# Kernel tuning notes

Measured on AMD Instinct MI355X. Metric: run time of the kernel, lower is better.

Reference implementation:

```python
import jax, jax.numpy as jnp
import numpy as np

SLOPE = 0.2  # LeakyReLU negative slope
EPS = 1e-8


def setup_inputs() -> dict:
    key = jax.random.key(0)
    ks = jax.random.split(key, 10)
    B, LL, D, H = 16, 257, 64, 128
    in_dim = D + 1  # lags=1 -> lags*D + 1
    sc = 0.1
    return {
        "x": jax.random.normal(ks[0], (B, LL, D), dtype=jnp.float32),
        "W1": jax.random.normal(ks[1], (D, H, in_dim), dtype=jnp.float32) * sc,
        "b1": jax.random.normal(ks[2], (D, H), dtype=jnp.float32) * sc,
        "W2": jax.random.normal(ks[3], (D, H, H), dtype=jnp.float32) * sc,
        "b2": jax.random.normal(ks[4], (D, H), dtype=jnp.float32) * sc,
        "W3": jax.random.normal(ks[5], (D, H, H), dtype=jnp.float32) * sc,
        "b3": jax.random.normal(ks[6], (D, H), dtype=jnp.float32) * sc,
        "W4": jax.random.normal(ks[7], (D, 1, H), dtype=jnp.float32) * sc,
        "b4": jax.random.normal(ks[8], (D, 1), dtype=jnp.float32) * sc,
        "lags": 1,
    }


def _forward(x, W1, b1, W2, b2, W3, b3, W4, b4, lags):
    B, LL, D = x.shape
    length = LL - lags
    # sliding windows of size lags+1 along time: [B, length, lags+1, D]
    windows = jnp.stack([x[:, i:i + length] for i in range(lags + 1)], axis=2)
    N = B * length
    x_lags = windows[:, :, :-1].reshape(N, lags * D)  # [N, lags*D]
    x_t = windows[:, :, -1].reshape(N, D)             # [N, D]

    def per_latent(w1, bb1, w2, bb2, w3, bb3, w4, bb4, xti):
        inp = jnp.concatenate([x_lags, xti[:, None]], axis=-1)  # [N, lags*D+1]
        p1 = inp @ w1.T + bb1
        s1 = jnp.where(p1 > 0, 1.0, SLOPE)
        a1 = p1 * s1
        p2 = a1 @ w2.T + bb2
        s2 = jnp.where(p2 > 0, 1.0, SLOPE)
        a2 = p2 * s2
        p3 = a2 @ w3.T + bb3
        s3 = jnp.where(p3 > 0, 1.0, SLOPE)
        a3 = p3 * s3
        out = a3 @ w4.T + bb4  # [N, 1]
        # analytic d out / d x_{t,i} (Jacobian diagonal): chain through LeakyReLU slopes
        d = s1 * w1[:, -1]      # [N, H]
        d = s2 * (d @ w2.T)     # [N, H]
        d = s3 * (d @ w3.T)     # [N, H]
        deriv = d @ w4[0]       # [N]
        return out[:, 0], deriv

    res, deriv = jax.vmap(per_latent, in_axes=(0, 0, 0, 0, 0, 0, 0, 0, 1))(
        W1, b1, W2, b2, W3, b3, W4, b4, x_t)  # res, deriv: [D, N]
    residuals = res.T.reshape(B, length, D)
    log_abs_det = jnp.log(jnp.abs(deriv) + EPS).sum(axis=0).reshape(B, length)
    return residuals, log_abs_det


def reference(x, W1, b1, W2, b2, W3, b3, W4, b4, lags):
    return _forward(x, W1, b1, W2, b2, W3, b3, W4, b4, lags)
```

## Files before the change

kernel.cpp:

```cpp
#include <hip/hip_runtime.h>
#include <hip/hip_bf16.h>
#include <math.h>

typedef _Float16 f16;
typedef _Float16 f16x8 __attribute__((ext_vector_type(8)));
typedef _Float16 f16x4 __attribute__((ext_vector_type(4)));
typedef float f32x4 __attribute__((ext_vector_type(4)));

#define MFMA(a, b, c) __builtin_amdgcn_mfma_f32_16x16x32_f16((a), (b), (c), 0, 0, 0)

constexpr int Dd = 64;
constexpr int Hh = 128;
constexpr int Nn = 4096;
constexpr int NT = 32;
constexpr float SLP = 0.2f;
constexpr float INV2K = 1.0f / 2048.0f;

constexpr int PD = 81920;
constexpr size_t W1L_OFF = (size_t)Dd * PD * 2;
constexpr size_t WS_NEEDED = W1L_OFF + (size_t)Dd * Hh * 4;

__device__ __forceinline__ int swz(int r, int c) {
  return (r << 7) + ((((c >> 3) ^ (r & 15)) << 3) | (c & 7));
}
__device__ __forceinline__ int swzK64(int r, int c) {
  return (r << 6) + (((((c >> 3) ^ r) & 7) << 3) | (c & 7));
}
__device__ __forceinline__ int swzF(int n, int h) {
  return (n << 7) + ((((h >> 2) ^ n) & 31) << 2) + (h & 3);
}

struct HL { f16 h, l; };
__device__ __forceinline__ HL split(float v) {
  HL r;
  r.h = (f16)v;
  r.l = (f16)((v - (float)r.h) * 2048.0f);
  return r;
}

__device__ __forceinline__ void cp_lds_async512(const void* g, void* l, int nbytes, int tid) {
  const int lane = tid & 63, wv = tid >> 6;
  for (int base = wv * 1024; base < nbytes; base += 8192) {
    __builtin_amdgcn_global_load_lds(
        (const __attribute__((address_space(1))) void*)((const char*)g + base + lane * 16),
        (__attribute__((address_space(3))) void*)((char*)l + base), 16, 0, 0);
  }
}

__global__ __launch_bounds__(256)
void prep_kernel(const float* __restrict__ W1, const float* __restrict__ W2,
                 const float* __restrict__ W3, f16* __restrict__ wsf,
                 float* __restrict__ w1lg, float* __restrict__ out_log) {
  const int gid = blockIdx.x * 256 + threadIdx.x;
  if (gid < Dd * Hh) w1lg[gid] = W1[(gid >> 7) * 8320 + (gid & 127) * 65 + 64];
  if (gid < Nn) out_log[gid] = 0.f;

  const int d = gid / 10240;
  const int r = gid - d * 10240;
  f16* outd = wsf + (size_t)d * PD;
  float vv[8];
  f16* dst;
  int plane;
  if (r < 2048) {
    int rem = r & 1023;
    int hf = r >> 10;
    plane = rem >> 9;
    int j = rem & 511;
    int row = j >> 3, sc = j & 7;
    int h = hf * 64 + row;
    int k0 = (sc ^ (row & 7)) << 3;
    const float* src = W1 + d * 8320 + h * 65 + k0;
#pragma unroll
    for (int e = 0; e < 8; e++) vv[e] = src[e];
    dst = outd + r * 8;
  } else {
    int r2 = r - 2048;
    int wsec = r2 >> 11;
    int rr = r2 & 2047;
    plane = rr >> 10;
    int j = rr & 1023;
    int row = j >> 4, sc = j & 15;
    int k0 = (sc ^ (row & 15)) << 3;
    const float* base = (wsec < 2 ? W2 : W3) + d * 16384 + (wsec & 1) * 8192;
    const float* src = base + row * 128 + k0;
    float4 v0 = *(const float4*)src, v1 = *(const float4*)(src + 4);
    vv[0] = v0.x; vv[1] = v0.y; vv[2] = v0.z; vv[3] = v0.w;
    vv[4] = v1.x; vv[5] = v1.y; vv[6] = v1.z; vv[7] = v1.w;
    dst = outd + 16384 + (wsec >> 1) * 32768 + (wsec & 1) * 16384 + rr * 8;
  }
  if (plane) {
#pragma unroll
    for (int e = 0; e < 8; e++) {
      f16 hi = (f16)vv[e];
      vv[e] = (vv[e] - (float)hi) * 2048.0f;
    }
  }
  f16x8 o;
#pragma unroll
  for (int e = 0; e < 8; e++) o[e] = (f16)vv[e];
  *(f16x8*)dst = o;
}

__device__ __forceinline__ void mid_phase(const f16* wb,
                                          const f16x8* axh, const f16x8* axl,
                                          const f16x8* ayh, const f16x8* ayl,
                                          int hr, int quad,
                                          f32x4& aP, f32x4& aS, f32x4& dP, f32x4& dS) {
#pragma unroll
  for (int kc = 0; kc < 4; kc++) {
    int ko = kc * 32 + quad * 8;
    f16x8 wh = *(const f16x8*)&wb[swz(hr, ko)];
    f16x8 wl = *(const f16x8*)&wb[8192 + swz(hr, ko)];
    aP = MFMA(wh, axh[kc], aP);
    aS = MFMA(wl, axh[kc], aS);
    aS = MFMA(wh, axl[kc], aS);
    dP = MFMA(wh, ayh[kc], dP);
    dS = MFMA(wl, ayh[kc], dS);
    dS = MFMA(wh, ayl[kc], dS);
  }
}

__global__ __launch_bounds__(512, 4)
void np_prior_fast(const float* __restrict__ x, const f16* __restrict__ wsw,
                   const float* __restrict__ w1lg,
                   const float* __restrict__ b1, const float* __restrict__ b2,
                   const float* __restrict__ b3, const float* __restrict__ W4,
                   const float* __restrict__ b4,
                   float* __restrict__ out_res, float* __restrict__ out_log) {
  __shared__ float4 smem[4096];
  f16* AH = (f16*)smem;
  f16* AL = AH + NT * 128;
  f16* DH = AL + NT * 128;
  f16* DL = DH + NT * 128;
  f16* Wreg = (f16*)((char*)smem + 32768);
  float* A3F = (float*)smem;
  float* D3F = (float*)((char*)smem + 16384);

  const int tid = threadIdx.x, d = blockIdx.y, n0 = blockIdx.x * NT;
  const int lane = tid & 63, wv = tid >> 6, l15 = lane & 15, quad = lane >> 4;
  const int nt = wv & 1, wq = wv >> 1;
  const int ra = nt * 16 + l15;
  const int hr = wq * 16 + l15;

  const f16* wd = wsw + (size_t)d * PD;
  const float* w1l = w1lg + d * Hh;
  const float* b1d = b1 + d * Hh;
  const f32x4 zero = {0.f, 0.f, 0.f, 0.f};

  cp_lds_async512(wd, Wreg, 32768, tid);
  {
    int n = tid >> 4, k4 = (tid & 15) << 2;
    int ng = n0 + n, bb = ng >> 8, tt = ng & 255;
    float4 v = *(const float4*)&x[(bb * 257 + tt) * 64 + k4];
    HL a = split(v.x), b = split(v.y), c = split(v.z), e = split(v.w);
    int o = swz(n, k4);
    *(f16x4*)&AH[o] = f16x4{a.h, b.h, c.h, e.h};
    *(f16x4*)&AL[o] = f16x4{a.l, b.l, c.l, e.l};
  }
  float xtv;
  {
    int ng = n0 + ra, bb = ng >> 8, tt = ng & 255;
    xtv = x[(bb * 257 + tt + 1) * 64 + d];
  }
  __syncthreads();

  f32x4 l1P[2], l1S[2];
  {
    f16x8 l1xh[2], l1xl[2];
#pragma unroll
    for (int kc = 0; kc < 2; kc++) {
      int ko = kc * 32 + quad * 8;
      l1xh[kc] = *(const f16x8*)&AH[swz(ra, ko)];
      l1xl[kc] = *(const f16x8*)&AL[swz(ra, ko)];
    }
#pragma unroll
    for (int hf = 0; hf < 2; hf++) {
      const f16* wb = Wreg + hf * 8192;
      l1P[hf] = zero; l1S[hf] = zero;
#pragma unroll
      for (int kc = 0; kc < 2; kc++) {
        int ko = kc * 32 + quad * 8;
        f16x8 wh = *(const f16x8*)&wb[swzK64(hr, ko)];
        f16x8 wl = *(const f16x8*)&wb[4096 + swzK64(hr, ko)];
        l1P[hf] = MFMA(wh, l1xh[kc], l1P[hf]);
        l1S[hf] = MFMA(wl, l1xh[kc], l1S[hf]);
        l1S[hf] = MFMA(wh, l1xl[kc], l1S[hf]);
      }
    }
  }
  __syncthreads();
  cp_lds_async512(wd + 16384, Wreg, 32768, tid);

#pragma unroll
  for (int hf = 0; hf < 2; hf++) {
    int hb = hf * 64 + wq * 16 + quad * 4;
    float4 wv4 = *(const float4*)&w1l[hb];
    float4 bv4 = *(const float4*)&b1d[hb];
    f16x4 ah, al, dh, dl;
#pragma unroll
    for (int j = 0; j < 4; j++) {
      float w1j = (&wv4.x)[j];
      float p = l1P[hf][j] + l1S[hf][j] * INV2K + xtv * w1j + (&bv4.x)[j];
      float s = p > 0.f ? 1.f : SLP;
      HL av = split(p * s), dv = split(s * w1j);
      ah[j] = av.h; al[j] = av.l; dh[j] = dv.h; dl[j] = dv.l;
    }
    int o = swz(ra, hb);
    *(f16x4*)&AH[o] = ah; *(f16x4*)&AL[o] = al;
    *(f16x4*)&DH[o] = dh; *(f16x4*)&DL[o] = dl;
  }
  __syncthreads();

  f32x4 aP[2], aS[2], dP[2], dS[2];
  {
    f16x8 axh[4], axl[4], ayh[4], ayl[4];
#pragma unroll
    for (int kc = 0; kc < 4; kc++) {
      int ko = kc * 32 + quad * 8;
      axh[kc] = *(const f16x8*)&AH[swz(ra, ko)];
      axl[kc] = *(const f16x8*)&AL[swz(ra, ko)];
      ayh[kc] = *(const f16x8*)&DH[swz(ra, ko)];
      ayl[kc] = *(const f16x8*)&DL[swz(ra, ko)];
    }
#pragma unroll
    for (int hf = 0; hf < 2; hf++) {
      if (hf == 1) {
        __syncthreads();
        cp_lds_async512(wd + 32768, Wreg, 32768, tid);
        __syncthreads();
      }
      aP[hf] = zero; aS[hf] = zero; dP[hf] = zero; dS[hf] = zero;
      mid_phase(Wreg, axh, axl, ayh, ayl, hr, quad,
                aP[hf], aS[hf], dP[hf], dS[hf]);
    }
  }
  __syncthreads();
  cp_lds_async512(wd + 49152, Wreg, 32768, tid);

  {
    const float* b2d = b2 + d * Hh;
#pragma unroll
    for (int hf = 0; hf < 2; hf++) {
      int hb = hf * 64 + wq * 16 + quad * 4;
      float4 bv4 = *(const float4*)&b2d[hb];
      f16x4 ah, al, dh, dl;
#pragma unroll
      for (int j = 0; j < 4; j++) {
        float p = aP[hf][j] + aS[hf][j] * INV2K + (&bv4.x)[j];
        float s = p > 0.f ? 1.f : SLP;
        float dd = s * (dP[hf][j] + dS[hf][j] * INV2K);
        HL av = split(p * s), dv = split(dd);
        ah[j] = av.h; al[j] = av.l; dh[j] = dv.h; dl[j] = dv.l;
      }
      int o = swz(ra, hb);
      *(f16x4*)&AH[o] = ah; *(f16x4*)&AL[o] = al;
      *(f16x4*)&DH[o] = dh; *(f16x4*)&DL[o] = dl;
    }
  }
  __syncthreads();

  {
    f16x8 axh[4], axl[4], ayh[4], ayl[4];
#pragma unroll
    for (int kc = 0; kc < 4; kc++) {
      int ko = kc * 32 + quad * 8;
      axh[kc] = *(const f16x8*)&AH[swz(ra, ko)];
      axl[kc] = *(const f16x8*)&AL[swz(ra, ko)];
      ayh[kc] = *(const f16x8*)&DH[swz(ra, ko)];
      ayl[kc] = *(const f16x8*)&DL[swz(ra, ko)];
    }
#pragma unroll
    for (int hf = 0; hf < 2; hf++) {
      if (hf == 1) {
        __syncthreads();
        cp_lds_async512(wd + 65536, Wreg, 32768, tid);
        __syncthreads();
      }
      aP[hf] = zero; aS[hf] = zero; dP[hf] = zero; dS[hf] = zero;
      mid_phase(Wreg, axh, axl, ayh, ayl, hr, quad,
                aP[hf], aS[hf], dP[hf], dS[hf]);
    }
  }
  __syncthreads();

  {
    const float* b3d = b3 + d * Hh;
#pragma unroll
    for (int hf = 0; hf < 2; hf++) {
      int hb = hf * 64 + wq * 16 + quad * 4;
      float4 bv4 = *(const float4*)&b3d[hb];
      float4 pa, pd;
#pragma unroll
      for (int j = 0; j < 4; j++) {
        float p = aP[hf][j] + aS[hf][j] * INV2K + (&bv4.x)[j];
        float s = p > 0.f ? 1.f : SLP;
        (&pa.x)[j] = p * s;
        (&pd.x)[j] = s * (dP[hf][j] + dS[hf][j] * INV2K);
      }
      *(float4*)&A3F[swzF(ra, hb)] = pa;
      *(float4*)&D3F[swzF(ra, hb)] = pd;
    }
  }
  __syncthreads();

  {
    int n = tid >> 4, g16 = tid & 15;
    const float* w4d = W4 + d * Hh;
    int c = g16 * 8;
    float4 va0 = *(const float4*)&A3F[swzF(n, c)];
    float4 va1 = *(const float4*)&A3F[swzF(n, c + 4)];
    float4 vd0 = *(const float4*)&D3F[swzF(n, c)];
    float4 vd1 = *(const float4*)&D3F[swzF(n, c + 4)];
    float4 w0 = *(const float4*)&w4d[c];
    float4 w1 = *(const float4*)&w4d[c + 4];
    float sr = va0.x * w0.x + va0.y * w0.y + va0.z * w0.z + va0.w * w0.w +
               va1.x * w1.x + va1.y * w1.y + va1.z * w1.z + va1.w * w1.w;
    float sd = vd0.x * w0.x + vd0.y * w0.y + vd0.z * w0.z + vd0.w * w0.w +
               vd1.x * w1.x + vd1.y * w1.y + vd1.z * w1.z + vd1.w * w1.w;
    sr += __shfl_xor(sr, 1); sr += __shfl_xor(sr, 2);
    sr += __shfl_xor(sr, 4); sr += __shfl_xor(sr, 8);
    sd += __shfl_xor(sd, 1); sd += __shfl_xor(sd, 2);
    sd += __shfl_xor(sd, 4); sd += __shfl_xor(sd, 8);
    if (g16 == 0) {
      int ng = n0 + n;
      out_res[ng * 64 + d] = sr + b4[d];
      atomicAdd(&out_log[ng], logf(fabsf(sd) + 1e-8f));
    }
  }
}

__device__ __forceinline__ void stage_wf(f16* WH, f16* WL,
                                         const float* __restrict__ g, int tid) {
  for (int i = tid; i < 2048; i += 256) {
    int h = i >> 5, k4 = (i & 31) << 2;
    float4 v = ((const float4*)g)[i];
    HL a = split(v.x), b = split(v.y), c = split(v.z), e = split(v.w);
    int o = swz(h, k4);
    *(f16x4*)&WH[o] = f16x4{a.h, b.h, c.h, e.h};
    *(f16x4*)&WL[o] = f16x4{a.l, b.l, c.l, e.l};
  }
}

__device__ __forceinline__ void mid_mfma_half(
    const f16* AH, const f16* AL, const f16* DH, const f16* DL,
    const f16* WH, const f16* WL, int nt, int wq, int l15, int quad,
    f32x4* aP, f32x4* aS, f32x4* dP, f32x4* dS) {
#pragma unroll
  for (int kc = 0; kc < 4; kc++) {
    int ko = kc * 32 + quad * 8;
    int ra = nt * 16 + l15;
    f16x8 xh = *(const f16x8*)&AH[swz(ra, ko)];
    f16x8 xl = *(const f16x8*)&AL[swz(ra, ko)];
    f16x8 yh = *(const f16x8*)&DH[swz(ra, ko)];
    f16x8 yl = *(const f16x8*)&DL[swz(ra, ko)];
#pragma unroll
    for (int c2 = 0; c2 < 2; c2++) {
      int hr = (2 * wq + c2) * 16 + l15;
      f16x8 wh = *(const f16x8*)&WH[swz(hr, ko)];
      f16x8 wl = *(const f16x8*)&WL[swz(hr, ko)];
      aP[c2] = MFMA(wh, xh, aP[c2]);
      aS[c2] = MFMA(wl, xh, aS[c2]);
      aS[c2] = MFMA(wh, xl, aS[c2]);
      dP[c2] = MFMA(wh, yh, dP[c2]);
      dS[c2] = MFMA(wl, yh, dS[c2]);
      dS[c2] = MFMA(wh, yl, dS[c2]);
    }
  }
}

__global__ __launch_bounds__(256, 2)
void np_prior_fb(const float* __restrict__ x,
                 const float* __restrict__ W1, const float* __restrict__ b1,
                 const float* __restrict__ W2, const float* __restrict__ b2,
                 const float* __restrict__ W3, const float* __restrict__ b3,
                 const float* __restrict__ W4, const float* __restrict__ b4,
                 float* __restrict__ out_res, float* __restrict__ out_log) {
  __shared__ float4 smem[4096];
  f16* AH = (f16*)smem;
  f16* AL = AH + NT * 128;
  f16* DH = AL + NT * 128;
  f16* DL = DH + NT * 128;
  f16* WHp = (f16*)((char*)smem + 32768);
  f16* WLp = WHp + 64 * 128;
  float* A3F = (float*)smem;
  float* D3F = (float*)((char*)smem + 16384);

  const int tid = threadIdx.x, d = blockIdx.y, n0 = blockIdx.x * NT;
  const int lane = tid & 63, wv = tid >> 6, l15 = lane & 15, quad = lane >> 4;
  const int nt = wv & 1, wq = wv >> 1;

  const float* W1d = W1 + d * Hh * 65;
  const float* b1d = b1 + d * Hh;
  const f32x4 zero = {0.f, 0.f, 0.f, 0.f};

  for (int i = tid; i < NT * 16; i += 256) {
    int n = i >> 4, k4 = (i & 15) << 2;
    int ng = n0 + n, bb = ng >> 8, tt = ng & 255;
    float4 v = *(const float4*)&x[(bb * 257 + tt) * 64 + k4];
    HL a = split(v.x), b = split(v.y), c = split(v.z), e = split(v.w);
    int o = swz(n, k4);
    *(f16x4*)&AH[o] = f16x4{a.h, b.h, c.h, e.h};
    *(f16x4*)&AL[o] = f16x4{a.l, b.l, c.l, e.l};
  }
  float xtv;
  {
    int ng = n0 + nt * 16 + l15, bb = ng >> 8, tt = ng & 255;
    xtv = x[(bb * 257 + tt + 1) * 64 + d];
  }
  for (int i = tid; i < 64 * 64; i += 256) {
    int h = i >> 6, k = i & 63;
    HL s = split(W1d[h * 65 + k]);
    int o = swz(h, k);
    WHp[o] = s.h; WLp[o] = s.l;
  }
  __syncthreads();

  f32x4 l1P[2][2], l1S[2][2];
  for (int hf = 0; hf < 2; hf++) {
    if (hf == 1) {
      __syncthreads();
      for (int i = tid; i < 64 * 64; i += 256) {
        int h = i >> 6, k = i & 63;
        HL s = split(W1d[(64 + h) * 65 + k]);
        int o = swz(h, k);
        WHp[o] = s.h; WLp[o] = s.l;
      }
      __syncthreads();
    }
    l1P[hf][0] = zero; l1P[hf][1] = zero;
    l1S[hf][0] = zero; l1S[hf][1] = zero;
#pragma unroll
    for (int kc = 0; kc < 2; kc++) {
      int ko = kc * 32 + quad * 8;
      f16x8 xh = *(const f16x8*)&AH[swz(nt * 16 + l15, ko)];
      f16x8 xl = *(const f16x8*)&AL[swz(nt * 16 + l15, ko)];
#pragma unroll
      for (int c2 = 0; c2 < 2; c2++) {
        int hr = (2 * wq + c2) * 16 + l15;
        f16x8 wh = *(const f16x8*)&WHp[swz(hr, ko)];
        f16x8 wl = *(const f16x8*)&WLp[swz(hr, ko)];
        l1P[hf][c2] = MFMA(wh, xh, l1P[hf][c2]);
        l1S[hf][c2] = MFMA(wl, xh, l1S[hf][c2]);
        l1S[hf][c2] = MFMA(wh, xl, l1S[hf][c2]);
      }
    }
  }
  __syncthreads();

  {
    int n = nt * 16 + l15;
#pragma unroll
    for (int hf = 0; hf < 2; hf++)
#pragma unroll
      for (int c2 = 0; c2 < 2; c2++) {
        int hb = hf * 64 + (2 * wq + c2) * 16 + quad * 4;
        f16x4 ah, al, dh, dl;
#pragma unroll
        for (int j = 0; j < 4; j++) {
          int h = hb + j;
          float w1j = W1d[h * 65 + 64];
          float p = l1P[hf][c2][j] + l1S[hf][c2][j] * INV2K + xtv * w1j + b1d[h];
          float s = p > 0.f ? 1.f : SLP;
          HL av = split(p * s), dv = split(s * w1j);
          ah[j] = av.h; al[j] = av.l; dh[j] = dv.h; dl[j] = dv.l;
        }
        int o = swz(n, hb);
        *(f16x4*)&AH[o] = ah; *(f16x4*)&AL[o] = al;
        *(f16x4*)&DH[o] = dh; *(f16x4*)&DL[o] = dl;
      }
  }
  stage_wf(WHp, WLp, W2 + d * Hh * Hh, tid);
  __syncthreads();

  f32x4 aP[2][2], aS[2][2], dP[2][2], dS[2][2];
  for (int hf = 0; hf < 2; hf++) {
    if (hf == 1) {
      __syncthreads();
      stage_wf(WHp, WLp, W2 + d * Hh * Hh + 64 * 128, tid);
      __syncthreads();
    }
    aP[hf][0] = zero; aP[hf][1] = zero; aS[hf][0] = zero; aS[hf][1] = zero;
    dP[hf][0] = zero; dP[hf][1] = zero; dS[hf][0] = zero; dS[hf][1] = zero;
    mid_mfma_half(AH, AL, DH, DL, WHp, WLp, nt, wq, l15, quad,
                  aP[hf], aS[hf], dP[hf], dS[hf]);
  }
  __syncthreads();

  {
    const float* b2d = b2 + d * Hh;
    int n = nt * 16 + l15;
#pragma unroll
    for (int hf = 0; hf < 2; hf++)
#pragma unroll
      for (int c2 = 0; c2 < 2; c2++) {
        int hb = hf * 64 + (2 * wq + c2) * 16 + quad * 4;
        f16x4 ah, al, dh, dl;
#pragma unroll
        for (int j = 0; j < 4; j++) {
          int h = hb + j;
          float p = aP[hf][c2][j] + aS[hf][c2][j] * INV2K + b2d[h];
          float s = p > 0.f ? 1.f : SLP;
          float dd = s * (dP[hf][c2][j] + dS[hf][c2][j] * INV2K);
          HL av = split(p * s), dv = split(dd);
          ah[j] = av.h; al[j] = av.l; dh[j] = dv.h; dl[j] = dv.l;
        }
        int o = swz(n, hb);
        *(f16x4*)&AH[o] = ah; *(f16x4*)&AL[o] = al;
        *(f16x4*)&DH[o] = dh; *(f16x4*)&DL[o] = dl;
      }
  }
  stage_wf(WHp, WLp, W3 + d * Hh * Hh, tid);
  __syncthreads();

  for (int hf = 0; hf < 2; hf++) {
    if (hf == 1) {
      __syncthreads();
      stage_wf(WHp, WLp, W3 + d * Hh * Hh + 64 * 128, tid);
      __syncthreads();
    }
    aP[hf][0] = zero; aP[hf][1] = zero; aS[hf][0] = zero; aS[hf][1] = zero;
    dP[hf][0] = zero; dP[hf][1] = zero; dS[hf][0] = zero; dS[hf][1] = zero;
    mid_mfma_half(AH, AL, DH, DL, WHp, WLp, nt, wq, l15, quad,
                  aP[hf], aS[hf], dP[hf], dS[hf]);
  }
  __syncthreads();

  {
    const float* b3d = b3 + d * Hh;
    int n = nt * 16 + l15;
#pragma unroll
    for (int hf = 0; hf < 2; hf++)
#pragma unroll
      for (int c2 = 0; c2 < 2; c2++) {
        int hb = hf * 64 + (2 * wq + c2) * 16 + quad * 4;
        float4 pa, pd;
#pragma unroll
        for (int j = 0; j < 4; j++) {
          int h = hb + j;
          float p = aP[hf][c2][j] + aS[hf][c2][j] * INV2K + b3d[h];
          float s = p > 0.f ? 1.f : SLP;
          (&pa.x)[j] = p * s;
          (&pd.x)[j] = s * (dP[hf][c2][j] + dS[hf][c2][j] * INV2K);
        }
        *(float4*)&A3F[swzF(n, hb)] = pa;
        *(float4*)&D3F[swzF(n, hb)] = pd;
      }
  }
  __syncthreads();

  {
    int n = tid >> 3, oct = tid & 7;
    const float* w4d = W4 + d * Hh;
    float sr = 0.f, sd = 0.f;
#pragma unroll
    for (int i = 0; i < 4; i++) {
      int c = oct * 16 + i * 4;
      float4 va = *(const float4*)&A3F[swzF(n, c)];
      float4 vd = *(const float4*)&D3F[swzF(n, c)];
      float4 w = *(const float4*)&w4d[c];
      sr += va.x * w.x + va.y * w.y + va.z * w.z + va.w * w.w;
      sd += vd.x * w.x + vd.y * w.y + vd.z * w.z + vd.w * w.w;
    }
    sr += __shfl_xor(sr, 1); sr += __shfl_xor(sr, 2); sr += __shfl_xor(sr, 4);
    sd += __shfl_xor(sd, 1); sd += __shfl_xor(sd, 2); sd += __shfl_xor(sd, 4);
    if (oct == 0) {
      int ng = n0 + n;
      out_res[ng * 64 + d] = sr + b4[d];
      atomicAdd(&out_log[ng], logf(fabsf(sd) + 1e-8f));
    }
  }
}

extern "C" void kernel_launch(void* const* d_in, const int* in_sizes, int n_in,
                              void* d_out, int out_size, void* d_ws, size_t ws_size,
                              hipStream_t stream) {
  (void)in_sizes; (void)n_in; (void)out_size;
  const float* x  = (const float*)d_in[0];
  const float* W1 = (const float*)d_in[1];
  const float* b1 = (const float*)d_in[2];
  const float* W2 = (const float*)d_in[3];
  const float* b2 = (const float*)d_in[4];
  const float* W3 = (const float*)d_in[5];
  const float* b3 = (const float*)d_in[6];
  const float* W4 = (const float*)d_in[7];
  const float* b4 = (const float*)d_in[8];

  float* out_res = (float*)d_out;
  float* out_log = out_res + Nn * Dd;

  if (ws_size >= WS_NEEDED) {
    f16* wsf = (f16*)d_ws;
    float* w1lg = (float*)((char*)d_ws + W1L_OFF);
    prep_kernel<<<2560, 256, 0, stream>>>(W1, W2, W3, wsf, w1lg, out_log);
    dim3 grid(Nn / NT, Dd);
    np_prior_fast<<<grid, 512, 0, stream>>>(x, wsf, w1lg, b1, b2, b3, W4, b4,
                                            out_res, out_log);
  } else {
    hipMemsetAsync(out_log, 0, Nn * sizeof(float), stream);
    dim3 grid(Nn / NT, Dd);
    np_prior_fb<<<grid, 256, 0, stream>>>(x, W1, b1, W2, b2, W3, b3, W4, b4,
                                          out_res, out_log);
  }
}
```

Baseline: 228.4 us.

## Add 64-row, 1024-thread variant with double-buffered weight staging in LDS

Adds a new kernel that handles 64 rows per block with 1024 threads and 96KB of dynamic LDS, so each weight load is shared by twice as many rows. The second weight half of each middle layer now loads into the activation region while the first half is multiplied, removing one barrier-separated load stall per layer. The new kernel runs when raising the dynamic shared memory limit succeeds and otherwise falls back to the old one. The costs are fewer resident blocks per CU and more threads waiting at each barrier.

Result: slower. 236.7 us (+3.6%).

```diff
diff --git a/kernel.cpp b/kernel.cpp
--- a/kernel.cpp
+++ b/kernel.cpp
@@ -41,6 +41,15 @@
 __device__ __forceinline__ void cp_lds_async512(const void* g, void* l, int nbytes, int tid) {
   const int lane = tid & 63, wv = tid >> 6;
   for (int base = wv * 1024; base < nbytes; base += 8192) {
+    __builtin_amdgcn_global_load_lds(
+        (const __attribute__((address_space(1))) void*)((const char*)g + base + lane * 16),
+        (__attribute__((address_space(3))) void*)((char*)l + base), 16, 0, 0);
+  }
+}
+
+__device__ __forceinline__ void cp_lds_async1024(const void* g, void* l, int nbytes, int tid) {
+  const int lane = tid & 63, wv = tid >> 6;
+  for (int base = wv * 1024; base < nbytes; base += 16384) {
     __builtin_amdgcn_global_load_lds(
         (const __attribute__((address_space(1))) void*)((const char*)g + base + lane * 16),
         (__attribute__((address_space(3))) void*)((char*)l + base), 16, 0, 0);
@@ -120,25 +129,26 @@
   }
 }
 
-__global__ __launch_bounds__(512, 4)
-void np_prior_fast(const float* __restrict__ x, const f16* __restrict__ wsw,
-                   const float* __restrict__ w1lg,
-                   const float* __restrict__ b1, const float* __restrict__ b2,
-                   const float* __restrict__ b3, const float* __restrict__ W4,
-                   const float* __restrict__ b4,
-                   float* __restrict__ out_res, float* __restrict__ out_log) {
-  __shared__ float4 smem[4096];
-  f16* AH = (f16*)smem;
-  f16* AL = AH + NT * 128;
-  f16* DH = AL + NT * 128;
-  f16* DL = DH + NT * 128;
-  f16* Wreg = (f16*)((char*)smem + 32768);
-  float* A3F = (float*)smem;
-  float* D3F = (float*)((char*)smem + 16384);
-
-  const int tid = threadIdx.x, d = blockIdx.y, n0 = blockIdx.x * NT;
+__global__ __launch_bounds__(1024, 4)
+void np_prior_f64(const float* __restrict__ x, const f16* __restrict__ wsw,
+                  const float* __restrict__ w1lg,
+                  const float* __restrict__ b1, const float* __restrict__ b2,
+                  const float* __restrict__ b3, const float* __restrict__ W4,
+                  const float* __restrict__ b4,
+                  float* __restrict__ out_res, float* __restrict__ out_log) {
+  extern __shared__ char dsm[];
+  f16* AH = (f16*)dsm;
+  f16* AL = AH + 8192;
+  f16* DH = AL + 8192;
+  f16* DL = DH + 8192;
+  f16* R0W = AH;
+  f16* Wreg = (f16*)(dsm + 65536);
+  float* A3F = (float*)dsm;
+  float* D3F = (float*)(dsm + 32768);
+
+  const int tid = threadIdx.x, d = blockIdx.y, n0 = blockIdx.x * 64;
   const int lane = tid & 63, wv = tid >> 6, l15 = lane & 15, quad = lane >> 4;
-  const int nt = wv & 1, wq = wv >> 1;
+  const int nt = wv & 3, wq = wv >> 2;
   const int ra = nt * 16 + l15;
   const int hr = wq * 16 + l15;
 
@@ -147,7 +157,7 @@
   const float* b1d = b1 + d * Hh;
   const f32x4 zero = {0.f, 0.f, 0.f, 0.f};
 
-  cp_lds_async512(wd, Wreg, 32768, tid);
+  cp_lds_async1024(wd, Wreg, 32768, tid);
   {
     int n = tid >> 4, k4 = (tid & 15) << 2;
     int ng = n0 + n, bb = ng >> 8, tt = ng & 255;
@@ -189,7 +199,7 @@
     }
   }
   __syncthreads();
-  cp_lds_async512(wd + 16384, Wreg, 32768, tid);
+  cp_lds_async1024(wd + 16384, Wreg, 32768, tid);
 
 #pragma unroll
   for (int hf = 0; hf < 2; hf++) {
@@ -222,20 +232,16 @@
       ayh[kc] = *(const f16x8*)&DH[swz(ra, ko)];
       ayl[kc] = *(const f16x8*)&DL[swz(ra, ko)];
     }
-#pragma unroll
-    for (int hf = 0; hf < 2; hf++) {
-      if (hf == 1) {
-        __syncthreads();
-        cp_lds_async512(wd + 32768, Wreg, 32768, tid);
-        __syncthreads();
-      }
-      aP[hf] = zero; aS[hf] = zero; dP[hf] = zero; dS[hf] = zero;
-      mid_phase(Wreg, axh, axl, ayh, ayl, hr, quad,
-                aP[hf], aS[hf], dP[hf], dS[hf]);
-    }
-  }
-  __syncthreads();
-  cp_lds_async512(wd + 49152, Wreg, 32768, tid);
+    __syncthreads();
+    cp_lds_async1024(wd + 32768, R0W, 32768, tid);
+    aP[0] = zero; aS[0] = zero; dP[0] = zero; dS[0] = zero;
+    mid_phase(Wreg, axh, axl, ayh, ayl, hr, quad, aP[0], aS[0], dP[0], dS[0]);
+    __syncthreads();
+    aP[1] = zero; aS[1] = zero; dP[1] = zero; dS[1] = zero;
+    mid_phase(R0W, axh, axl, ayh, ayl, hr, quad, aP[1], aS[1], dP[1], dS[1]);
+  }
+  __syncthreads();
+  cp_lds_async1024(wd + 49152, Wreg, 32768, tid);
 
   {
     const float* b2d = b2 + d * Hh;
@@ -269,17 +275,13 @@
       ayh[kc] = *(const f16x8*)&DH[swz(ra, ko)];
       ayl[kc] = *(const f16x8*)&DL[swz(ra, ko)];
     }
-#pragma unroll
-    for (int hf = 0; hf < 2; hf++) {
-      if (hf == 1) {
-        __syncthreads();
-        cp_lds_async512(wd + 65536, Wreg, 32768, tid);
-        __syncthreads();
-      }
-      aP[hf] = zero; aS[hf] = zero; dP[hf] = zero; dS[hf] = zero;
-      mid_phase(Wreg, axh, axl, ayh, ayl, hr, quad,
-                aP[hf], aS[hf], dP[hf], dS[hf]);
-    }
+    __syncthreads();
+    cp_lds_async1024(wd + 65536, R0W, 32768, tid);
+    aP[0] = zero; aS[0] = zero; dP[0] = zero; dS[0] = zero;
+    mid_phase(Wreg, axh, axl, ayh, ayl, hr, quad, aP[0], aS[0], dP[0], dS[0]);
+    __syncthreads();
+    aP[1] = zero; aS[1] = zero; dP[1] = zero; dS[1] = zero;
+    mid_phase(R0W, axh, axl, ayh, ayl, hr, quad, aP[1], aS[1], dP[1], dS[1]);
   }
   __syncthreads();
 
@@ -329,6 +331,215 @@
   }
 }
 
+__global__ __launch_bounds__(512, 4)
+void np_prior_fast(const float* __restrict__ x, const f16* __restrict__ wsw,
+                   const float* __restrict__ w1lg,
+                   const float* __restrict__ b1, const float* __restrict__ b2,
+                   const float* __restrict__ b3, const float* __restrict__ W4,
+                   const float* __restrict__ b4,
+                   float* __restrict__ out_res, float* __restrict__ out_log) {
+  __shared__ float4 smem[4096];
+  f16* AH = (f16*)smem;
+  f16* AL = AH + NT * 128;
+  f16* DH = AL + NT * 128;
+  f16* DL = DH + NT * 128;
+  f16* Wreg = (f16*)((char*)smem + 32768);
+  float* A3F = (float*)smem;
+  float* D3F = (float*)((char*)smem + 16384);
+
+  const int tid = threadIdx.x, d = blockIdx.y, n0 = blockIdx.x * NT;
+  const int lane = tid & 63, wv = tid >> 6, l15 = lane & 15, quad = lane >> 4;
+  const int nt = wv & 1, wq = wv >> 1;
+  const int ra = nt * 16 + l15;
+  const int hr = wq * 16 + l15;
+
+  const f16* wd = wsw + (size_t)d * PD;
+  const float* w1l = w1lg + d * Hh;
+  const float* b1d = b1 + d * Hh;
+  const f32x4 zero = {0.f, 0.f, 0.f, 0.f};
+
+  cp_lds_async512(wd, Wreg, 32768, tid);
+  {
+    int n = tid >> 4, k4 = (tid & 15) << 2;
+    int ng = n0 + n, bb = ng >> 8, tt = ng & 255;
+    float4 v = *(const float4*)&x[(bb * 257 + tt) * 64 + k4];
+    HL a = split(v.x), b = split(v.y), c = split(v.z), e = split(v.w);
+    int o = swz(n, k4);
+    *(f16x4*)&AH[o] = f16x4{a.h, b.h, c.h, e.h};
+    *(f16x4*)&AL[o] = f16x4{a.l, b.l, c.l, e.l};
+  }
+  float xtv;
+  {
+    int ng = n0 + ra, bb = ng >> 8, tt = ng & 255;
+    xtv = x[(bb * 257 + tt + 1) * 64 + d];
+  }
+  __syncthreads();
+
+  f32x4 l1P[2], l1S[2];
+  {
+    f16x8 l1xh[2], l1xl[2];
+#pragma unroll
+    for (int kc = 0; kc < 2; kc++) {
+      int ko = kc * 32 + quad * 8;
+      l1xh[kc] = *(const f16x8*)&AH[swz(ra, ko)];
+      l1xl[kc] = *(const f16x8*)&AL[swz(ra, ko)];
+    }
+#pragma unroll
+    for (int hf = 0; hf < 2; hf++) {
+      const f16* wb = Wreg + hf * 8192;
+      l1P[hf] = zero; l1S[hf] = zero;
+#pragma unroll
+      for (int kc = 0; kc < 2; kc++) {
+        int ko = kc * 32 + quad * 8;
+        f16x8 wh = *(const f16x8*)&wb[swzK64(hr, ko)];
+        f16x8 wl = *(const f16x8*)&wb[4096 + swzK64(hr, ko)];
+        l1P[hf] = MFMA(wh, l1xh[kc], l1P[hf]);
+        l1S[hf] = MFMA(wl, l1xh[kc], l1S[hf]);
+        l1S[hf] = MFMA(wh, l1xl[kc], l1S[hf]);
+      }
+    }
+  }
+  __syncthreads();
+  cp_lds_async512(wd + 16384, Wreg, 32768, tid);
+
+#pragma unroll
+  for (int hf = 0; hf < 2; hf++) {
+    int hb = hf * 64 + wq * 16 + quad * 4;
+    float4 wv4 = *(const float4*)&w1l[hb];
+    float4 bv4 = *(const float4*)&b1d[hb];
+    f16x4 ah, al, dh, dl;
+#pragma unroll
+    for (int j = 0; j < 4; j++) {
+      float w1j = (&wv4.x)[j];
+      float p = l1P[hf][j] + l1S[hf][j] * INV2K + xtv * w1j + (&bv4.x)[j];
+      float s = p > 0.f ? 1.f : SLP;
+      HL av = split(p * s), dv = split(s * w1j);
+      ah[j] = av.h; al[j] = av.l; dh[j] = dv.h; dl[j] = dv.l;
+    }
+    int o = swz(ra, hb);
+    *(f16x4*)&AH[o] = ah; *(f16x4*)&AL[o] = al;
+    *(f16x4*)&DH[o] = dh; *(f16x4*)&DL[o] = dl;
+  }
+  __syncthreads();
+
+  f32x4 aP[2], aS[2], dP[2], dS[2];
+  {
+    f16x8 axh[4], axl[4], ayh[4], ayl[4];
+#pragma unroll
+    for (int kc = 0; kc < 4; kc++) {
+      int ko = kc * 32 + quad * 8;
+      axh[kc] = *(const f16x8*)&AH[swz(ra, ko)];
+      axl[kc] = *(const f16x8*)&AL[swz(ra, ko)];
+      ayh[kc] = *(const f16x8*)&DH[swz(ra, ko)];
+      ayl[kc] = *(const f16x8*)&DL[swz(ra, ko)];
+    }
+#pragma unroll
+    for (int hf = 0; hf < 2; hf++) {
+      if (hf == 1) {
+        __syncthreads();
+        cp_lds_async512(wd + 32768, Wreg, 32768, tid);
+        __syncthreads();
+      }
+      aP[hf] = zero; aS[hf] = zero; dP[hf] = zero; dS[hf] = zero;
+      mid_phase(Wreg, axh, axl, ayh, ayl, hr, quad,
+                aP[hf], aS[hf], dP[hf], dS[hf]);
+    }
+  }
+  __syncthreads();
+  cp_lds_async512(wd + 49152, Wreg, 32768, tid);
+
+  {
+    const float* b2d = b2 + d * Hh;
+#pragma unroll
+    for (int hf = 0; hf < 2; hf++) {
+      int hb = hf * 64 + wq * 16 + quad * 4;
+      float4 bv4 = *(const float4*)&b2d[hb];
+      f16x4 ah, al, dh, dl;
+#pragma unroll
+      for (int j = 0; j < 4; j++) {
+        float p = aP[hf][j] + aS[hf][j] * INV2K + (&bv4.x)[j];
+        float s = p > 0.f ? 1.f : SLP;
+        float dd = s * (dP[hf][j] + dS[hf][j] * INV2K);
+        HL av = split(p * s), dv = split(dd);
+        ah[j] = av.h; al[j] = av.l; dh[j] = dv.h; dl[j] = dv.l;
+      }
+      int o = swz(ra, hb);
+      *(f16x4*)&AH[o] = ah; *(f16x4*)&AL[o] = al;
+      *(f16x4*)&DH[o] = dh; *(f16x4*)&DL[o] = dl;
+    }
+  }
+  __syncthreads();
+
+  {
+    f16x8 axh[4], axl[4], ayh[4], ayl[4];
+#pragma unroll
+    for (int kc = 0; kc < 4; kc++) {
+      int ko = kc * 32 + quad * 8;
+      axh[kc] = *(const f16x8*)&AH[swz(ra, ko)];
+      axl[kc] = *(const f16x8*)&AL[swz(ra, ko)];
+      ayh[kc] = *(const f16x8*)&DH[swz(ra, ko)];
+      ayl[kc] = *(const f16x8*)&DL[swz(ra, ko)];
+    }
+#pragma unroll
+    for (int hf = 0; hf < 2; hf++) {
+      if (hf == 1) {
+        __syncthreads();
+        cp_lds_async512(wd + 65536, Wreg, 32768, tid);
+        __syncthreads();
+      }
+      aP[hf] = zero; aS[hf] = zero; dP[hf] = zero; dS[hf] = zero;
+      mid_phase(Wreg, axh, axl, ayh, ayl, hr, quad,
+                aP[hf], aS[hf], dP[hf], dS[hf]);
+    }
+  }
+  __syncthreads();
+
+  {
+    const float* b3d = b3 + d * Hh;
+#pragma unroll
+    for (int hf = 0; hf < 2; hf++) {
+      int hb = hf * 64 + wq * 16 + quad * 4;
+      float4 bv4 = *(const float4*)&b3d[hb];
+      float4 pa, pd;
+#pragma unroll
+      for (int j = 0; j < 4; j++) {
+        float p = aP[hf][j] + aS[hf][j] * INV2K + (&bv4.x)[j];
+        float s = p > 0.f ? 1.f : SLP;
+        (&pa.x)[j] = p * s;
+        (&pd.x)[j] = s * (dP[hf][j] + dS[hf][j] * INV2K);
+      }
+      *(float4*)&A3F[swzF(ra, hb)] = pa;
+      *(float4*)&D3F[swzF(ra, hb)] = pd;
+    }
+  }
+  __syncthreads();
+
+  {
+    int n = tid >> 4, g16 = tid & 15;
+    const float* w4d = W4 + d * Hh;
+    int c = g16 * 8;
+    float4 va0 = *(const float4*)&A3F[swzF(n, c)];
+    float4 va1 = *(const float4*)&A3F[swzF(n, c + 4)];
+    float4 vd0 = *(const float4*)&D3F[swzF(n, c)];
+    float4 vd1 = *(const float4*)&D3F[swzF(n, c + 4)];
+    float4 w0 = *(const float4*)&w4d[c];
+    float4 w1 = *(const float4*)&w4d[c + 4];
+    float sr = va0.x * w0.x + va0.y * w0.y + va0.z * w0.z + va0.w * w0.w +
+               va1.x * w1.x + va1.y * w1.y + va1.z * w1.z + va1.w * w1.w;
+    float sd = vd0.x * w0.x + vd0.y * w0.y + vd0.z * w0.z + vd0.w * w0.w +
+               vd1.x * w1.x + vd1.y * w1.y + vd1.z * w1.z + vd1.w * w1.w;
+    sr += __shfl_xor(sr, 1); sr += __shfl_xor(sr, 2);
+    sr += __shfl_xor(sr, 4); sr += __shfl_xor(sr, 8);
+    sd += __shfl_xor(sd, 1); sd += __shfl_xor(sd, 2);
+    sd += __shfl_xor(sd, 4); sd += __shfl_xor(sd, 8);
+    if (g16 == 0) {
+      int ng = n0 + n;
+      out_res[ng * 64 + d] = sr + b4[d];
+      atomicAdd(&out_log[ng], logf(fabsf(sd) + 1e-8f));
+    }
+  }
+}
+
 __device__ __forceinline__ void stage_wf(f16* WH, f16* WL,
                                          const float* __restrict__ g, int tid) {
   for (int i = tid; i < 2048; i += 256) {
@@ -588,13 +799,29 @@
   float* out_res = (float*)d_out;
   float* out_log = out_res + Nn * Dd;
 
+  static int big_lds = -1;
+  if (big_lds < 0) {
+    big_lds = (hipFuncSetAttribute(
+                   (const void*)np_prior_f64,
+                   hipFuncAttributeMaxDynamicSharedMemorySize, 98304) ==
+               hipSuccess)
+                  ? 1
+                  : 0;
+  }
+
   if (ws_size >= WS_NEEDED) {
     f16* wsf = (f16*)d_ws;
     float* w1lg = (float*)((char*)d_ws + W1L_OFF);
     prep_kernel<<<2560, 256, 0, stream>>>(W1, W2, W3, wsf, w1lg, out_log);
-    dim3 grid(Nn / NT, Dd);
-    np_prior_fast<<<grid, 512, 0, stream>>>(x, wsf, w1lg, b1, b2, b3, W4, b4,
-                                            out_res, out_log);
+    if (big_lds == 1) {
+      dim3 grid(Nn / 64, Dd);
+      np_prior_f64<<<grid, 1024, 98304, stream>>>(x, wsf, w1lg, b1, b2, b3,
+                                                  W4, b4, out_res, out_log);
+    } else {
+      dim3 grid(Nn / NT, Dd);
+      np_prior_fast<<<grid, 512, 0, stream>>>(x, wsf, w1lg, b1, b2, b3, W4,
+                                              b4, out_res, out_log);
+    }
   } else {
     hipMemsetAsync(out_log, 0, Nn * sizeof(float), stream);
     dim3 grid(Nn / NT, Dd);
```

## Double row tile to 64 and stream weights in 32-row chunks

Applied to the files above, without the earlier changes.

Each block now handles 64 rows instead of 32, with 8 waves split as 4 row tiles by 2 hidden-column groups. Weights are staged into LDS in smaller 32-output-row chunks, and the prep kernel lays them out to match. The layer activations are converted per chunk, and the buffer moves to 80KB of dynamic shared memory. This halves the number of blocks that reload the per-latent weights and so cuts weight traffic per row. The cost is more LDS per block, which lowers occupancy, and more barrier-separated chunk loads.

New measurement: 212.2 us. 1.08x faster.

```diff
diff --git a/kernel.cpp b/kernel.cpp
--- a/kernel.cpp
+++ b/kernel.cpp
@@ -75,18 +75,20 @@
     dst = outd + r * 8;
   } else {
     int r2 = r - 2048;
-    int wsec = r2 >> 11;
-    int rr = r2 & 2047;
-    plane = rr >> 10;
-    int j = rr & 1023;
+    int wmat = r2 >> 12;
+    int rr4 = r2 & 4095;
+    int chunk = rr4 >> 10;
+    int rr = rr4 & 1023;
+    plane = rr >> 9;
+    int j = rr & 511;
     int row = j >> 4, sc = j & 15;
     int k0 = (sc ^ (row & 15)) << 3;
-    const float* base = (wsec < 2 ? W2 : W3) + d * 16384 + (wsec & 1) * 8192;
-    const float* src = base + row * 128 + k0;
+    const float* srcb = (wmat == 0 ? W2 : W3) + d * 16384;
+    const float* src = srcb + (chunk * 32 + row) * 128 + k0;
     float4 v0 = *(const float4*)src, v1 = *(const float4*)(src + 4);
     vv[0] = v0.x; vv[1] = v0.y; vv[2] = v0.z; vv[3] = v0.w;
     vv[4] = v1.x; vv[5] = v1.y; vv[6] = v1.z; vv[7] = v1.w;
-    dst = outd + 16384 + (wsec >> 1) * 32768 + (wsec & 1) * 16384 + rr * 8;
+    dst = outd + 16384 + wmat * 32768 + chunk * 8192 + rr * 8;
   }
   if (plane) {
 #pragma unroll
@@ -101,16 +103,16 @@
   *(f16x8*)dst = o;
 }
 
-__device__ __forceinline__ void mid_phase(const f16* wb,
+__device__ __forceinline__ void mid_chunk(const f16* ws,
                                           const f16x8* axh, const f16x8* axl,
                                           const f16x8* ayh, const f16x8* ayl,
-                                          int hr, int quad,
+                                          int hrc, int quad,
                                           f32x4& aP, f32x4& aS, f32x4& dP, f32x4& dS) {
 #pragma unroll
   for (int kc = 0; kc < 4; kc++) {
     int ko = kc * 32 + quad * 8;
-    f16x8 wh = *(const f16x8*)&wb[swz(hr, ko)];
-    f16x8 wl = *(const f16x8*)&wb[8192 + swz(hr, ko)];
+    f16x8 wh = *(const f16x8*)&ws[swz(hrc, ko)];
+    f16x8 wl = *(const f16x8*)&ws[4096 + swz(hrc, ko)];
     aP = MFMA(wh, axh[kc], aP);
     aS = MFMA(wl, axh[kc], aS);
     aS = MFMA(wh, axl[kc], aS);
@@ -121,41 +123,48 @@
 }
 
 __global__ __launch_bounds__(512, 4)
-void np_prior_fast(const float* __restrict__ x, const f16* __restrict__ wsw,
-                   const float* __restrict__ w1lg,
-                   const float* __restrict__ b1, const float* __restrict__ b2,
-                   const float* __restrict__ b3, const float* __restrict__ W4,
-                   const float* __restrict__ b4,
-                   float* __restrict__ out_res, float* __restrict__ out_log) {
-  __shared__ float4 smem[4096];
-  f16* AH = (f16*)smem;
-  f16* AL = AH + NT * 128;
-  f16* DH = AL + NT * 128;
-  f16* DL = DH + NT * 128;
-  f16* Wreg = (f16*)((char*)smem + 32768);
-  float* A3F = (float*)smem;
-  float* D3F = (float*)((char*)smem + 16384);
-
-  const int tid = threadIdx.x, d = blockIdx.y, n0 = blockIdx.x * NT;
+void np_prior_v2(const float* __restrict__ x, const f16* __restrict__ wsw,
+                 const float* __restrict__ w1lg,
+                 const float* __restrict__ b1, const float* __restrict__ b2,
+                 const float* __restrict__ b3, const float* __restrict__ W4,
+                 const float* __restrict__ b4,
+                 float* __restrict__ out_res, float* __restrict__ out_log) {
+  extern __shared__ char dsm[];
+  f16* AH = (f16*)dsm;
+  f16* AL = AH + 8192;
+  f16* DH = AL + 8192;
+  f16* DL = DH + 8192;
+  f16* Ws = (f16*)(dsm + 65536);
+  float* A3F = (float*)dsm;
+  float* D3F = (float*)(dsm + 32768);
+
+  const int tid = threadIdx.x, d = blockIdx.y, n0 = blockIdx.x * 64;
   const int lane = tid & 63, wv = tid >> 6, l15 = lane & 15, quad = lane >> 4;
-  const int nt = wv & 1, wq = wv >> 1;
+  const int nt = wv & 3, wq = wv >> 2;
   const int ra = nt * 16 + l15;
-  const int hr = wq * 16 + l15;
+  const int hrc = wq * 16 + l15;
 
   const f16* wd = wsw + (size_t)d * PD;
   const float* w1l = w1lg + d * Hh;
   const float* b1d = b1 + d * Hh;
   const f32x4 zero = {0.f, 0.f, 0.f, 0.f};
 
-  cp_lds_async512(wd, Wreg, 32768, tid);
-  {
-    int n = tid >> 4, k4 = (tid & 15) << 2;
+  cp_lds_async512(wd, Ws, 16384, tid);
+  {
+    int n = tid >> 3, k8 = (tid & 7) << 3;
     int ng = n0 + n, bb = ng >> 8, tt = ng & 255;
-    float4 v = *(const float4*)&x[(bb * 257 + tt) * 64 + k4];
-    HL a = split(v.x), b = split(v.y), c = split(v.z), e = split(v.w);
-    int o = swz(n, k4);
-    *(f16x4*)&AH[o] = f16x4{a.h, b.h, c.h, e.h};
-    *(f16x4*)&AL[o] = f16x4{a.l, b.l, c.l, e.l};
+    const float* xs = &x[(bb * 257 + tt) * 64 + k8];
+    float4 v0 = *(const float4*)xs, v1 = *(const float4*)(xs + 4);
+    float va[8] = {v0.x, v0.y, v0.z, v0.w, v1.x, v1.y, v1.z, v1.w};
+    f16x8 vh, vl;
+#pragma unroll
+    for (int e = 0; e < 8; e++) {
+      HL s = split(va[e]);
+      vh[e] = s.h; vl[e] = s.l;
+    }
+    int o = swz(n, k8);
+    *(f16x8*)&AH[o] = vh;
+    *(f16x8*)&AL[o] = vl;
   }
   float xtv;
   {
@@ -164,54 +173,53 @@
   }
   __syncthreads();
 
-  f32x4 l1P[2], l1S[2];
-  {
-    f16x8 l1xh[2], l1xl[2];
-#pragma unroll
-    for (int kc = 0; kc < 2; kc++) {
-      int ko = kc * 32 + quad * 8;
-      l1xh[kc] = *(const f16x8*)&AH[swz(ra, ko)];
-      l1xl[kc] = *(const f16x8*)&AL[swz(ra, ko)];
-    }
-#pragma unroll
-    for (int hf = 0; hf < 2; hf++) {
-      const f16* wb = Wreg + hf * 8192;
-      l1P[hf] = zero; l1S[hf] = zero;
+  f16x8 l1xh[2], l1xl[2];
+#pragma unroll
+  for (int kc = 0; kc < 2; kc++) {
+    int ko = kc * 32 + quad * 8;
+    l1xh[kc] = *(const f16x8*)&AH[swz(ra, ko)];
+    l1xl[kc] = *(const f16x8*)&AL[swz(ra, ko)];
+  }
+#pragma unroll 1
+  for (int cf = 0; cf < 2; cf++) {
+    f32x4 P[2], S[2];
+#pragma unroll
+    for (int hf2 = 0; hf2 < 2; hf2++) {
+      int hr64 = hf2 * 32 + hrc;
+      P[hf2] = zero; S[hf2] = zero;
 #pragma unroll
       for (int kc = 0; kc < 2; kc++) {
         int ko = kc * 32 + quad * 8;
-        f16x8 wh = *(const f16x8*)&wb[swzK64(hr, ko)];
-        f16x8 wl = *(const f16x8*)&wb[4096 + swzK64(hr, ko)];
-        l1P[hf] = MFMA(wh, l1xh[kc], l1P[hf]);
-        l1S[hf] = MFMA(wl, l1xh[kc], l1S[hf]);
-        l1S[hf] = MFMA(wh, l1xl[kc], l1S[hf]);
-      }
-    }
-  }
-  __syncthreads();
-  cp_lds_async512(wd + 16384, Wreg, 32768, tid);
-
-#pragma unroll
-  for (int hf = 0; hf < 2; hf++) {
-    int hb = hf * 64 + wq * 16 + quad * 4;
-    float4 wv4 = *(const float4*)&w1l[hb];
-    float4 bv4 = *(const float4*)&b1d[hb];
-    f16x4 ah, al, dh, dl;
-#pragma unroll
-    for (int j = 0; j < 4; j++) {
-      float w1j = (&wv4.x)[j];
-      float p = l1P[hf][j] + l1S[hf][j] * INV2K + xtv * w1j + (&bv4.x)[j];
-      float s = p > 0.f ? 1.f : SLP;
-      HL av = split(p * s), dv = split(s * w1j);
-      ah[j] = av.h; al[j] = av.l; dh[j] = dv.h; dl[j] = dv.l;
-    }
-    int o = swz(ra, hb);
-    *(f16x4*)&AH[o] = ah; *(f16x4*)&AL[o] = al;
-    *(f16x4*)&DH[o] = dh; *(f16x4*)&DL[o] = dl;
-  }
-  __syncthreads();
-
-  f32x4 aP[2], aS[2], dP[2], dS[2];
+        f16x8 wh = *(const f16x8*)&Ws[swzK64(hr64, ko)];
+        f16x8 wl = *(const f16x8*)&Ws[4096 + swzK64(hr64, ko)];
+        P[hf2] = MFMA(wh, l1xh[kc], P[hf2]);
+        S[hf2] = MFMA(wl, l1xh[kc], S[hf2]);
+        S[hf2] = MFMA(wh, l1xl[kc], S[hf2]);
+      }
+    }
+    __syncthreads();
+    cp_lds_async512(wd + (cf == 0 ? 8192 : 16384), Ws, 16384, tid);
+#pragma unroll
+    for (int hf2 = 0; hf2 < 2; hf2++) {
+      int hb = cf * 64 + hf2 * 32 + wq * 16 + quad * 4;
+      float4 wv4 = *(const float4*)&w1l[hb];
+      float4 bv4 = *(const float4*)&b1d[hb];
+      f16x4 ah, al, dh, dl;
+#pragma unroll
+      for (int j = 0; j < 4; j++) {
+        float w1j = (&wv4.x)[j];
+        float p = P[hf2][j] + S[hf2][j] * INV2K + xtv * w1j + (&bv4.x)[j];
+        float s = p > 0.f ? 1.f : SLP;
+        HL av = split(p * s), dv = split(s * w1j);
+        ah[j] = av.h; al[j] = av.l; dh[j] = dv.h; dl[j] = dv.l;
+      }
+      int o = swz(ra, hb);
+      *(f16x4*)&AH[o] = ah; *(f16x4*)&AL[o] = al;
+      *(f16x4*)&DH[o] = dh; *(f16x4*)&DL[o] = dl;
+    }
+    __syncthreads();
+  }
+
   {
     f16x8 axh[4], axl[4], ayh[4], ayl[4];
 #pragma unroll
@@ -222,42 +230,37 @@
       ayh[kc] = *(const f16x8*)&DH[swz(ra, ko)];
       ayl[kc] = *(const f16x8*)&DL[swz(ra, ko)];
     }
-#pragma unroll
-    for (int hf = 0; hf < 2; hf++) {
-      if (hf == 1) {
+    __syncthreads();
+    const float* b2d = b2 + d * Hh;
+#pragma unroll 1
+    for (int c = 0; c < 4; c++) {
+      if (c > 0) {
         __syncthreads();
-        cp_lds_async512(wd + 32768, Wreg, 32768, tid);
+        cp_lds_async512(wd + 16384 + c * 8192, Ws, 16384, tid);
         __syncthreads();
       }
-      aP[hf] = zero; aS[hf] = zero; dP[hf] = zero; dS[hf] = zero;
-      mid_phase(Wreg, axh, axl, ayh, ayl, hr, quad,
-                aP[hf], aS[hf], dP[hf], dS[hf]);
-    }
-  }
-  __syncthreads();
-  cp_lds_async512(wd + 49152, Wreg, 32768, tid);
-
-  {
-    const float* b2d = b2 + d * Hh;
-#pragma unroll
-    for (int hf = 0; hf < 2; hf++) {
-      int hb = hf * 64 + wq * 16 + quad * 4;
-      float4 bv4 = *(const float4*)&b2d[hb];
-      f16x4 ah, al, dh, dl;
-#pragma unroll
-      for (int j = 0; j < 4; j++) {
-        float p = aP[hf][j] + aS[hf][j] * INV2K + (&bv4.x)[j];
-        float s = p > 0.f ? 1.f : SLP;
-        float dd = s * (dP[hf][j] + dS[hf][j] * INV2K);
-        HL av = split(p * s), dv = split(dd);
-        ah[j] = av.h; al[j] = av.l; dh[j] = dv.h; dl[j] = dv.l;
-      }
-      int o = swz(ra, hb);
-      *(f16x4*)&AH[o] = ah; *(f16x4*)&AL[o] = al;
-      *(f16x4*)&DH[o] = dh; *(f16x4*)&DL[o] = dl;
-    }
-  }
-  __syncthreads();
+      f32x4 aP = zero, aS = zero, dP = zero, dS = zero;
+      mid_chunk(Ws, axh, axl, ayh, ayl, hrc, quad, aP, aS, dP, dS);
+      {
+        int hb = c * 32 + wq * 16 + quad * 4;
+        float4 bv4 = *(const float4*)&b2d[hb];
+        f16x4 ah, al, dh, dl;
+#pragma unroll
+        for (int j = 0; j < 4; j++) {
+          float p = aP[j] + aS[j] * INV2K + (&bv4.x)[j];
+          float s = p > 0.f ? 1.f : SLP;
+          float dd = s * (dP[j] + dS[j] * INV2K);
+          HL av = split(p * s), dv = split(dd);
+          ah[j] = av.h; al[j] = av.l; dh[j] = dv.h; dl[j] = dv.l;
+        }
+        int o = swz(ra, hb);
+        *(f16x4*)&AH[o] = ah; *(f16x4*)&AL[o] = al;
+        *(f16x4*)&DH[o] = dh; *(f16x4*)&DL[o] = dl;
+      }
+    }
+  }
+  __syncthreads();
+  cp_lds_async512(wd + 49152, Ws, 16384, tid);
 
   {
     f16x8 axh[4], axl[4], ayh[4], ayl[4];
@@ -269,59 +272,51 @@
       ayh[kc] = *(const f16x8*)&DH[swz(ra, ko)];
       ayl[kc] = *(const f16x8*)&DL[swz(ra, ko)];
     }
-#pragma unroll
-    for (int hf = 0; hf < 2; hf++) {
-      if (hf == 1) {
+    __syncthreads();
+    const float* b3d = b3 + d * Hh;
+#pragma unroll 1
+    for (int c = 0; c < 4; c++) {
+      if (c > 0) {
         __syncthreads();
-        cp_lds_async512(wd + 65536, Wreg, 32768, tid);
+        cp_lds_async512(wd + 49152 + c * 8192, Ws, 16384, tid);
         __syncthreads();
       }
-      aP[hf] = zero; aS[hf] = zero; dP[hf] = zero; dS[hf] = zero;
-      mid_phase(Wreg, axh, axl, ayh, ayl, hr, quad,
-                aP[hf], aS[hf], dP[hf], dS[hf]);
-    }
-  }
-  __syncthreads();
-
-  {
-    const float* b3d = b3 + d * Hh;
-#pragma unroll
-    for (int hf = 0; hf < 2; hf++) {
-      int hb = hf * 64 + wq * 16 + quad * 4;
-      float4 bv4 = *(const float4*)&b3d[hb];
-      float4 pa, pd;
-#pragma unroll
-      for (int j = 0; j < 4; j++) {
-        float p = aP[hf][j] + aS[hf][j] * INV2K + (&bv4.x)[j];
-        float s = p > 0.f ? 1.f : SLP;
-        (&pa.x)[j] = p * s;
-        (&pd.x)[j] = s * (dP[hf][j] + dS[hf][j] * INV2K);
-      }
-      *(float4*)&A3F[swzF(ra, hb)] = pa;
-      *(float4*)&D3F[swzF(ra, hb)] = pd;
-    }
-  }
-  __syncthreads();
-
-  {
-    int n = tid >> 4, g16 = tid & 15;
+      f32x4 aP = zero, aS = zero, dP = zero, dS = zero;
+      mid_chunk(Ws, axh, axl, ayh, ayl, hrc, quad, aP, aS, dP, dS);
+      {
+        int hb = c * 32 + wq * 16 + quad * 4;
+        float4 bv4 = *(const float4*)&b3d[hb];
+        float4 pa, pd;
+#pragma unroll
+        for (int j = 0; j < 4; j++) {
+          float p = aP[j] + aS[j] * INV2K + (&bv4.x)[j];
+          float s = p > 0.f ? 1.f : SLP;
+          (&pa.x)[j] = p * s;
+          (&pd.x)[j] = s * (dP[j] + dS[j] * INV2K);
+        }
+        *(float4*)&A3F[swzF(ra, hb)] = pa;
+        *(float4*)&D3F[swzF(ra, hb)] = pd;
+      }
+    }
+  }
+  __syncthreads();
+
+  {
+    int n = tid >> 3, oct = tid & 7;
     const float* w4d = W4 + d * Hh;
-    int c = g16 * 8;
-    float4 va0 = *(const float4*)&A3F[swzF(n, c)];
-    float4 va1 = *(const float4*)&A3F[swzF(n, c + 4)];
-    float4 vd0 = *(const float4*)&D3F[swzF(n, c)];
-    float4 vd1 = *(const float4*)&D3F[swzF(n, c + 4)];
-    float4 w0 = *(const float4*)&w4d[c];
-    float4 w1 = *(const float4*)&w4d[c + 4];
-    float sr = va0.x * w0.x + va0.y * w0.y + va0.z * w0.z + va0.w * w0.w +
-               va1.x * w1.x + va1.y * w1.y + va1.z * w1.z + va1.w * w1.w;
-    float sd = vd0.x * w0.x + vd0.y * w0.y + vd0.z * w0.z + vd0.w * w0.w +
-               vd1.x * w1.x + vd1.y * w1.y + vd1.z * w1.z + vd1.w * w1.w;
-    sr += __shfl_xor(sr, 1); sr += __shfl_xor(sr, 2);
-    sr += __shfl_xor(sr, 4); sr += __shfl_xor(sr, 8);
-    sd += __shfl_xor(sd, 1); sd += __shfl_xor(sd, 2);
-    sd += __shfl_xor(sd, 4); sd += __shfl_xor(sd, 8);
-    if (g16 == 0) {
+    float sr = 0.f, sd = 0.f;
+#pragma unroll
+    for (int i = 0; i < 4; i++) {
+      int c = oct * 16 + i * 4;
+      float4 va = *(const float4*)&A3F[swzF(n, c)];
+      float4 vd = *(const float4*)&D3F[swzF(n, c)];
+      float4 w = *(const float4*)&w4d[c];
+      sr += va.x * w.x + va.y * w.y + va.z * w.z + va.w * w.w;
+      sd += vd.x * w.x + vd.y * w.y + vd.z * w.z + vd.w * w.w;
+    }
+    sr += __shfl_xor(sr, 1); sr += __shfl_xor(sr, 2); sr += __shfl_xor(sr, 4);
+    sd += __shfl_xor(sd, 1); sd += __shfl_xor(sd, 2); sd += __shfl_xor(sd, 4);
+    if (oct == 0) {
       int ng = n0 + n;
       out_res[ng * 64 + d] = sr + b4[d];
       atomicAdd(&out_log[ng], logf(fabsf(sd) + 1e-8f));
@@ -588,13 +583,23 @@
   float* out_res = (float*)d_out;
   float* out_log = out_res + Nn * Dd;
 
-  if (ws_size >= WS_NEEDED) {
+  static int big_lds = -1;
+  if (big_lds < 0) {
+    big_lds = (hipFuncSetAttribute(
+                   (const void*)np_prior_v2,
+                   hipFuncAttributeMaxDynamicSharedMemorySize, 81920) ==
+               hipSuccess)
+                  ? 1
+                  : 0;
+  }
+
+  if (ws_size >= WS_NEEDED && big_lds == 1) {
     f16* wsf = (f16*)d_ws;
     float* w1lg = (float*)((char*)d_ws + W1L_OFF);
     prep_kernel<<<2560, 256, 0, stream>>>(W1, W2, W3, wsf, w1lg, out_log);
-    dim3 grid(Nn / NT, Dd);
-    np_prior_fast<<<grid, 512, 0, stream>>>(x, wsf, w1lg, b1, b2, b3, W4, b4,
-                                            out_res, out_log);
+    dim3 grid(Nn / 64, Dd);
+    np_prior_v2<<<grid, 512, 81920, stream>>>(x, wsf, w1lg, b1, b2, b3, W4,
+                                              b4, out_res, out_log);
   } else {
     hipMemsetAsync(out_log, 0, Nn * sizeof(float), stream);
     dim3 grid(Nn / NT, Dd);
```
